# Kernel tuning notes

Hardware: AMD Instinct MI355X
Metric: run time of the kernel (lower is better)

## Reference

```python
import jax, jax.numpy as jnp
import numpy as np

N_QUBITS = 4
N_LAYERS = 3
N_FEATURES = 64
BATCH = 524288


def setup_inputs() -> dict:
    key = jax.random.key(0)
    k1, k2, k3, k4 = jax.random.split(key, 4)
    x = jax.random.normal(k1, (BATCH, N_FEATURES), jnp.float32)
    # nn.Linear(64, 4) params
    lim = 1.0 / np.sqrt(N_FEATURES)
    W_pre = jax.random.uniform(k2, (N_QUBITS, N_FEATURES), jnp.float32, -lim, lim)
    b_pre = jax.random.uniform(k3, (N_QUBITS,), jnp.float32, -lim, lim)
    # quantum circuit weights: randn * 0.1
    qweights = jax.random.normal(k4, (N_LAYERS, N_QUBITS, 2), jnp.float32) * 0.1
    return {"x": x, "W_pre": W_pre, "b_pre": b_pre, "qweights": qweights}


def _coef(theta, n):
    # reshape scalar or [B] angle to broadcast against [B, 2,..,2] (n-1 trailing dims after slicing)
    return jnp.reshape(theta, (-1,) + (1,) * (n - 1))


def _apply_ry(state, wire, theta):
    # RY(t) = [[cos t/2, -sin t/2], [sin t/2, cos t/2]] applied on `wire`
    n = state.ndim - 1
    s = jnp.moveaxis(state, 1 + wire, -1)
    a, b = s[..., 0], s[..., 1]
    c = _coef(jnp.cos(theta / 2), n)
    sn = _coef(jnp.sin(theta / 2), n)
    out = jnp.stack([c * a - sn * b, sn * a + c * b], axis=-1)
    return jnp.moveaxis(out, -1, 1 + wire)


def _apply_rz(state, wire, theta):
    # RZ(t) = diag(e^{-i t/2}, e^{+i t/2})
    n = state.ndim - 1
    s = jnp.moveaxis(state, 1 + wire, -1)
    half = _coef(theta / 2, n)
    out = jnp.stack([jnp.exp(-1j * half) * s[..., 0],
                     jnp.exp(1j * half) * s[..., 1]], axis=-1)
    return jnp.moveaxis(out, -1, 1 + wire)


def _apply_cnot(state, ctrl, tgt):
    s = jnp.moveaxis(state, (1 + ctrl, 1 + tgt), (-2, -1))
    s = jnp.concatenate([s[..., 0:1, :], s[..., 1:2, ::-1]], axis=-2)
    return jnp.moveaxis(s, (-2, -1), (1 + ctrl, 1 + tgt))


def _circuit(angles, qweights):
    # batched 4-qubit statevector simulation; state shape [B, 2,2,2,2] (wire 0 = MSB)
    B, n = angles.shape
    nl = qweights.shape[0]
    state = jnp.zeros((B,) + (2,) * n, jnp.complex64)
    state = state.at[(slice(None),) + (0,) * n].set(1.0)
    for w in range(n):
        state = _apply_ry(state, w, angles[:, w])
    for l in range(nl):
        for w in range(n):
            state = _apply_ry(state, w, qweights[l, w, 0])
            state = _apply_rz(state, w, qweights[l, w, 1])
        for w in range(n):
            state = _apply_cnot(state, w, (w + 1) % n)
    probs = state.real ** 2 + state.imag ** 2  # [B, 2,2,2,2] float32
    exps = []
    for w in range(n):
        marg = jnp.moveaxis(probs, 1 + w, 1).reshape(B, 2, -1).sum(-1)  # [B, 2]
        exps.append(marg[:, 0] - marg[:, 1])  # <Z_w>
    return jnp.stack(exps, axis=1)  # [B, n]


def reference(x, W_pre, b_pre, qweights):
    angles = jnp.tanh(x @ W_pre.T + b_pre)  # [B, n_qubits]
    return _circuit(angles, qweights).astype(jnp.float32)
```

## Files before the change

### kernel.cpp

```cpp
#include <hip/hip_runtime.h>
#include <cmath>


#define BAR() asm volatile("s_waitcnt lgkmcnt(0)\n\ts_barrier" ::: "memory")

#define LOADX(R0, R1, R2, R3, P, C)                       \
  R0 = xb[((P) * 256 + 0 * 64) * 16 + (C) * 4];           \
  R1 = xb[((P) * 256 + 1 * 64) * 16 + (C) * 4];           \
  R2 = xb[((P) * 256 + 2 * 64) * 16 + (C) * 4];           \
  R3 = xb[((P) * 256 + 3 * 64) * 16 + (C) * 4];

#define STAGE(R0, R1, R2, R3)                                            \
  *reinterpret_cast<float4*>(&lds[(0 * 64 + rrow) * XS + q4w]) = R0;     \
  *reinterpret_cast<float4*>(&lds[(1 * 64 + rrow) * XS + q4w]) = R1;     \
  *reinterpret_cast<float4*>(&lds[(2 * 64 + rrow) * XS + q4w]) = R2;     \
  *reinterpret_cast<float4*>(&lds[(3 * 64 + rrow) * XS + q4w]) = R3;

#define GEMV(A0, A1, A2, A3, C) {                                          \
  const float4 xv0 = *reinterpret_cast<const float4*>(&lds[tid * XS + 0]); \
  const float4 xv1 = *reinterpret_cast<const float4*>(&lds[tid * XS + 4]); \
  const float4 xv2 = *reinterpret_cast<const float4*>(&lds[tid * XS + 8]); \
  const float4 xv3 = *reinterpret_cast<const float4*>(&lds[tid * XS + 12]);\
  const float xr[16] = {xv0.x, xv0.y, xv0.z, xv0.w, xv1.x, xv1.y, xv1.z,   \
                        xv1.w, xv2.x, xv2.y, xv2.z, xv2.w, xv3.x, xv3.y,   \
                        xv3.z, xv3.w};                                     \
  _Pragma("unroll")                                                        \
  for (int f = 0; f < 16; ++f) {                                          \
    A0 = fmaf(xr[f], Wp[(C) * 16 + f], A0);                                \
    A1 = fmaf(xr[f], Wp[64 + (C) * 16 + f], A1);                           \
    A2 = fmaf(xr[f], Wp[128 + (C) * 16 + f], A2);                          \
    A3 = fmaf(xr[f], Wp[192 + (C) * 16 + f], A3);                          \
  } }

__global__ __launch_bounds__(256) void qprep_kernel(
    const float* __restrict__ qw,
    float* __restrict__ A_out)
{
  __shared__ float sre[16][17];
  __shared__ float sim[16][17];
  __shared__ float M[4][16][16];
  const int tid = threadIdx.x;
  const int col = tid >> 4;
  const int u   = tid & 15;

  sre[col][u] = (u == col) ? 1.0f : 0.0f;
  sim[col][u] = 0.0f;
  __syncthreads();

#pragma unroll
  for (int l = 0; l < 3; ++l) {
#pragma unroll
    for (int w = 0; w < 4; ++w) {
      const int mask = 8 >> w;
      float sh, ch, sh2, ch2;
      __sincosf(0.5f * qw[(l * 4 + w) * 2 + 0], &sh, &ch);
      __sincosf(0.5f * qw[(l * 4 + w) * 2 + 1], &sh2, &ch2);
      const int ua = u & ~mask, ub = u | mask;
      const float ar = sre[col][ua], ai = sim[col][ua];
      const float br = sre[col][ub], bi = sim[col][ub];
      __syncthreads();
      float nr, ni;
      if (u & mask) { nr = sh * ar + ch * br; ni = sh * ai + ch * bi; }
      else          { nr = ch * ar - sh * br; ni = ch * ai - sh * bi; }
      float rr, ri;
      if (u & mask) { rr = ch2 * nr - sh2 * ni; ri = ch2 * ni + sh2 * nr; }
      else          { rr = ch2 * nr + sh2 * ni; ri = ch2 * ni - sh2 * nr; }
      sre[col][u] = rr; sim[col][u] = ri;
      __syncthreads();
    }
    int src = u;
    if (src & 1) src ^= 8;
    if (src & 2) src ^= 1;
    if (src & 4) src ^= 2;
    if (src & 8) src ^= 4;
    const float pr = sre[col][src], pi = sim[col][src];
    __syncthreads();
    sre[col][u] = pr; sim[col][u] = pi;
    __syncthreads();
  }

  for (int idx = tid; idx < 1024; idx += 256) {
    const int w = idx >> 8, s = (idx >> 4) & 15, t = idx & 15;
    const int mask = 8 >> w;
    float acc = 0.0f;
#pragma unroll
    for (int uu = 0; uu < 16; ++uu) {
      const float z = (uu & mask) ? -1.0f : 1.0f;
      acc += z * (sre[s][uu] * sre[t][uu] + sim[s][uu] * sim[t][uu]);
    }
    M[w >> 0][s][t] = acc;
  }
  __syncthreads();

  for (int idx = tid; idx < 324; idx += 256) {
    const int w = idx & 3, pq = idx >> 2;
    const int p = pq / 9, q = pq % 9;
    const int i0 = p / 3, i1 = p % 3, i2 = q / 3, i3 = q % 3;
    float acc = 0.0f;
#pragma unroll
    for (int comb = 0; comb < 16; ++comb) {
      int s = 0, t = 0;
      float coef = 0.0625f;
      int j;
      j = (comb >> 3) & 1; s |= j << 3; t |= ((i0 == 2) ? (j ^ 1) : j) << 3; if (i0 == 1 && j) coef = -coef;
      j = (comb >> 2) & 1; s |= j << 2; t |= ((i1 == 2) ? (j ^ 1) : j) << 2; if (i1 == 1 && j) coef = -coef;
      j = (comb >> 1) & 1; s |= j << 1; t |= ((i2 == 2) ? (j ^ 1) : j) << 1; if (i2 == 1 && j) coef = -coef;
      j = comb & 1;        s |= j;      t |= ((i3 == 2) ? (j ^ 1) : j);      if (i3 == 1 && j) coef = -coef;
      acc = fmaf(coef, M[w][s][t], acc);
    }
    A_out[idx] = acc;
  }
}

__global__ __launch_bounds__(256)
__attribute__((amdgpu_waves_per_eu(4, 4)))
void qmain_kernel(
    const float* __restrict__ x,
    const float* __restrict__ Wp,
    const float* __restrict__ bp,
    const float4* __restrict__ Aws,
    float* __restrict__ out)
{
  constexpr int XS = 20;
  __shared__ alignas(16) float lds[256 * XS];

  const int tid = threadIdx.x;
  const size_t row0 = (size_t)blockIdx.x * 512;
  const int rrow = tid >> 2;
  const int q4w  = (tid & 3) << 2;
  const float4* xb = reinterpret_cast<const float4*>(x) +
                     (row0 + (size_t)rrow) * 16 + (tid & 3);

  float4 rbA0, rbA1, rbA2, rbA3, rbB0, rbB1, rbB2, rbB3;
  LOADX(rbA0, rbA1, rbA2, rbA3, 0, 0);
  LOADX(rbB0, rbB1, rbB2, rbB3, 0, 1);

  float aA0 = 0.f, aA1 = 0.f, aA2 = 0.f, aA3 = 0.f;
  float aB0 = 0.f, aB1 = 0.f, aB2 = 0.f, aB3 = 0.f;

  STAGE(rbA0, rbA1, rbA2, rbA3); LOADX(rbA0, rbA1, rbA2, rbA3, 0, 2); BAR();
  GEMV(aA0, aA1, aA2, aA3, 0);   BAR();
  STAGE(rbB0, rbB1, rbB2, rbB3); LOADX(rbB0, rbB1, rbB2, rbB3, 0, 3); BAR();
  GEMV(aA0, aA1, aA2, aA3, 1);   BAR();
  STAGE(rbA0, rbA1, rbA2, rbA3); LOADX(rbA0, rbA1, rbA2, rbA3, 1, 0); BAR();
  GEMV(aA0, aA1, aA2, aA3, 2);   BAR();
  STAGE(rbB0, rbB1, rbB2, rbB3); LOADX(rbB0, rbB1, rbB2, rbB3, 1, 1); BAR();
  GEMV(aA0, aA1, aA2, aA3, 3);   BAR();
  STAGE(rbA0, rbA1, rbA2, rbA3); LOADX(rbA0, rbA1, rbA2, rbA3, 1, 2); BAR();
  GEMV(aB0, aB1, aB2, aB3, 0);   BAR();
  STAGE(rbB0, rbB1, rbB2, rbB3); LOADX(rbB0, rbB1, rbB2, rbB3, 1, 3); BAR();
  GEMV(aB0, aB1, aB2, aB3, 1);   BAR();
  STAGE(rbA0, rbA1, rbA2, rbA3); BAR();
  GEMV(aB0, aB1, aB2, aB3, 2);   BAR();
  STAGE(rbB0, rbB1, rbB2, rbB3); BAR();
  GEMV(aB0, aB1, aB2, aB3, 3);

  float g0[9], h0[9], g1[9], h1[9];
  {
    const float t0 = 1.0f - 2.0f / (__expf(2.0f * (aA0 + bp[0])) + 1.0f);
    const float t1 = 1.0f - 2.0f / (__expf(2.0f * (aA1 + bp[1])) + 1.0f);
    const float t2 = 1.0f - 2.0f / (__expf(2.0f * (aA2 + bp[2])) + 1.0f);
    const float t3 = 1.0f - 2.0f / (__expf(2.0f * (aA3 + bp[3])) + 1.0f);
    float c0, s0, c1, s1, c2, s2, c3, s3;
    __sincosf(t0, &s0, &c0); __sincosf(t1, &s1, &c1);
    __sincosf(t2, &s2, &c2); __sincosf(t3, &s3, &c3);
    g0[0] = 1.f; g0[1] = c1; g0[2] = s1; g0[3] = c0; g0[4] = c0 * c1;
    g0[5] = c0 * s1; g0[6] = s0; g0[7] = s0 * c1; g0[8] = s0 * s1;
    h0[0] = 1.f; h0[1] = c3; h0[2] = s3; h0[3] = c2; h0[4] = c2 * c3;
    h0[5] = c2 * s3; h0[6] = s2; h0[7] = s2 * c3; h0[8] = s2 * s3;
  }
  {
    const float t0 = 1.0f - 2.0f / (__expf(2.0f * (aB0 + bp[0])) + 1.0f);
    const float t1 = 1.0f - 2.0f / (__expf(2.0f * (aB1 + bp[1])) + 1.0f);
    const float t2 = 1.0f - 2.0f / (__expf(2.0f * (aB2 + bp[2])) + 1.0f);
    const float t3 = 1.0f - 2.0f / (__expf(2.0f * (aB3 + bp[3])) + 1.0f);
    float c0, s0, c1, s1, c2, s2, c3, s3;
    __sincosf(t0, &s0, &c0); __sincosf(t1, &s1, &c1);
    __sincosf(t2, &s2, &c2); __sincosf(t3, &s3, &c3);
    g1[0] = 1.f; g1[1] = c1; g1[2] = s1; g1[3] = c0; g1[4] = c0 * c1;
    g1[5] = c0 * s1; g1[6] = s0; g1[7] = s0 * c1; g1[8] = s0 * s1;
    h1[0] = 1.f; h1[1] = c3; h1[2] = s3; h1[3] = c2; h1[4] = c2 * c3;
    h1[5] = c2 * s3; h1[6] = s2; h1[7] = s2 * c3; h1[8] = s2 * s3;
  }

  float e00 = 0.f, e01 = 0.f, e02 = 0.f, e03 = 0.f;
  float e10 = 0.f, e11 = 0.f, e12 = 0.f, e13 = 0.f;
#pragma unroll
  for (int p = 0; p < 9; ++p) {
#pragma unroll
    for (int q = 0; q < 9; ++q) {
      const float4 a4 = Aws[p * 9 + q];
      const float tA = g0[p] * h0[q];
      const float tB = g1[p] * h1[q];
      e00 = fmaf(a4.x, tA, e00); e01 = fmaf(a4.y, tA, e01);
      e02 = fmaf(a4.z, tA, e02); e03 = fmaf(a4.w, tA, e03);
      e10 = fmaf(a4.x, tB, e10); e11 = fmaf(a4.y, tB, e11);
      e12 = fmaf(a4.z, tB, e12); e13 = fmaf(a4.w, tB, e13);
    }
  }
  float4* out4 = reinterpret_cast<float4*>(out);
  out4[row0 + tid]       = make_float4(e00, e01, e02, e03);
  out4[row0 + 256 + tid] = make_float4(e10, e11, e12, e13);
}

extern "C" void kernel_launch(void* const* d_in, const int* in_sizes, int n_in,
                              void* d_out, int out_size, void* d_ws, size_t ws_size,
                              hipStream_t stream) {
  const float* x  = (const float*)d_in[0];
  const float* Wp = (const float*)d_in[1];
  const float* bp = (const float*)d_in[2];
  const float* qw = (const float*)d_in[3];
  float* out = (float*)d_out;
  float* A = (float*)d_ws;
  (void)n_in; (void)out_size; (void)ws_size;

  qprep_kernel<<<1, 256, 0, stream>>>(qw, A);

  const int B = in_sizes[0] / 64;
  qmain_kernel<<<B / 512, 256, 0, stream>>>(x, Wp, bp,
                                            (const float4*)A, out);
}
```

Baseline: 38.27 us.

## Fuse circuit-precompute into main kernel, recomputing per block in LDS

Removes the separate single-block prep kernel and has every block recompute the 16x16 unitary, the observable matrices and the 324-entry coefficient table in shared memory while its first x loads are in flight. The prefetch depth grows from two to three register buffers so that more global loads overlap the prep. This drops one kernel launch and the serial dependency between the two kernels. In exchange, every block does redundant prep work with about 14 barriers, and register pressure rises under the fixed waves-per-EU setting.

```diff
diff --git a/kernel.cpp b/kernel.cpp
--- a/kernel.cpp
+++ b/kernel.cpp
@@ -32,97 +32,21 @@
     A3 = fmaf(xr[f], Wp[192 + (C) * 16 + f], A3);                          \
   } }
 
-__global__ __launch_bounds__(256) void qprep_kernel(
-    const float* __restrict__ qw,
-    float* __restrict__ A_out)
-{
-  __shared__ float sre[16][17];
-  __shared__ float sim[16][17];
-  __shared__ float M[4][16][16];
-  const int tid = threadIdx.x;
-  const int col = tid >> 4;
-  const int u   = tid & 15;
-
-  sre[col][u] = (u == col) ? 1.0f : 0.0f;
-  sim[col][u] = 0.0f;
-  __syncthreads();
-
-#pragma unroll
-  for (int l = 0; l < 3; ++l) {
-#pragma unroll
-    for (int w = 0; w < 4; ++w) {
-      const int mask = 8 >> w;
-      float sh, ch, sh2, ch2;
-      __sincosf(0.5f * qw[(l * 4 + w) * 2 + 0], &sh, &ch);
-      __sincosf(0.5f * qw[(l * 4 + w) * 2 + 1], &sh2, &ch2);
-      const int ua = u & ~mask, ub = u | mask;
-      const float ar = sre[col][ua], ai = sim[col][ua];
-      const float br = sre[col][ub], bi = sim[col][ub];
-      __syncthreads();
-      float nr, ni;
-      if (u & mask) { nr = sh * ar + ch * br; ni = sh * ai + ch * bi; }
-      else          { nr = ch * ar - sh * br; ni = ch * ai - sh * bi; }
-      float rr, ri;
-      if (u & mask) { rr = ch2 * nr - sh2 * ni; ri = ch2 * ni + sh2 * nr; }
-      else          { rr = ch2 * nr + sh2 * ni; ri = ch2 * ni - sh2 * nr; }
-      sre[col][u] = rr; sim[col][u] = ri;
-      __syncthreads();
-    }
-    int src = u;
-    if (src & 1) src ^= 8;
-    if (src & 2) src ^= 1;
-    if (src & 4) src ^= 2;
-    if (src & 8) src ^= 4;
-    const float pr = sre[col][src], pi = sim[col][src];
-    __syncthreads();
-    sre[col][u] = pr; sim[col][u] = pi;
-    __syncthreads();
-  }
-
-  for (int idx = tid; idx < 1024; idx += 256) {
-    const int w = idx >> 8, s = (idx >> 4) & 15, t = idx & 15;
-    const int mask = 8 >> w;
-    float acc = 0.0f;
-#pragma unroll
-    for (int uu = 0; uu < 16; ++uu) {
-      const float z = (uu & mask) ? -1.0f : 1.0f;
-      acc += z * (sre[s][uu] * sre[t][uu] + sim[s][uu] * sim[t][uu]);
-    }
-    M[w >> 0][s][t] = acc;
-  }
-  __syncthreads();
-
-  for (int idx = tid; idx < 324; idx += 256) {
-    const int w = idx & 3, pq = idx >> 2;
-    const int p = pq / 9, q = pq % 9;
-    const int i0 = p / 3, i1 = p % 3, i2 = q / 3, i3 = q % 3;
-    float acc = 0.0f;
-#pragma unroll
-    for (int comb = 0; comb < 16; ++comb) {
-      int s = 0, t = 0;
-      float coef = 0.0625f;
-      int j;
-      j = (comb >> 3) & 1; s |= j << 3; t |= ((i0 == 2) ? (j ^ 1) : j) << 3; if (i0 == 1 && j) coef = -coef;
-      j = (comb >> 2) & 1; s |= j << 2; t |= ((i1 == 2) ? (j ^ 1) : j) << 2; if (i1 == 1 && j) coef = -coef;
-      j = (comb >> 1) & 1; s |= j << 1; t |= ((i2 == 2) ? (j ^ 1) : j) << 1; if (i2 == 1 && j) coef = -coef;
-      j = comb & 1;        s |= j;      t |= ((i3 == 2) ? (j ^ 1) : j);      if (i3 == 1 && j) coef = -coef;
-      acc = fmaf(coef, M[w][s][t], acc);
-    }
-    A_out[idx] = acc;
-  }
-}
-
 __global__ __launch_bounds__(256)
 __attribute__((amdgpu_waves_per_eu(4, 4)))
-void qmain_kernel(
+void qfused_kernel(
     const float* __restrict__ x,
     const float* __restrict__ Wp,
     const float* __restrict__ bp,
-    const float4* __restrict__ Aws,
+    const float* __restrict__ qw,
     float* __restrict__ out)
 {
-  constexpr int XS = 20;
-  __shared__ alignas(16) float lds[256 * XS];
+  constexpr int XS  = 20;
+  constexpr int AOF = 256 * XS;
+  __shared__ alignas(16) float lds[256 * XS + 324];
+  constexpr int SRE = 0;
+  constexpr int SIM = 272;
+  constexpr int MOF = 544;
 
   const int tid = threadIdx.x;
   const size_t row0 = (size_t)blockIdx.x * 512;
@@ -131,28 +55,105 @@
   const float4* xb = reinterpret_cast<const float4*>(x) +
                      (row0 + (size_t)rrow) * 16 + (tid & 3);
 
-  float4 rbA0, rbA1, rbA2, rbA3, rbB0, rbB1, rbB2, rbB3;
-  LOADX(rbA0, rbA1, rbA2, rbA3, 0, 0);
-  LOADX(rbB0, rbB1, rbB2, rbB3, 0, 1);
+  float4 rA0, rA1, rA2, rA3, rB0, rB1, rB2, rB3, rC0, rC1, rC2, rC3;
+  LOADX(rA0, rA1, rA2, rA3, 0, 0);
+  LOADX(rB0, rB1, rB2, rB3, 0, 1);
+  LOADX(rC0, rC1, rC2, rC3, 0, 2);
+
+  {
+    const int col = tid >> 4;
+    const int u   = tid & 15;
+    lds[SRE + col * 17 + u] = (u == col) ? 1.0f : 0.0f;
+    lds[SIM + col * 17 + u] = 0.0f;
+    BAR();
+
+#pragma unroll
+    for (int l = 0; l < 3; ++l) {
+#pragma unroll
+      for (int w = 0; w < 4; ++w) {
+        const int mask = 8 >> w;
+        float sh, ch, sh2, ch2;
+        __sincosf(0.5f * qw[(l * 4 + w) * 2 + 0], &sh, &ch);
+        __sincosf(0.5f * qw[(l * 4 + w) * 2 + 1], &sh2, &ch2);
+        const int ua = u & ~mask, ub = u | mask;
+        const float ar = lds[SRE + col * 17 + ua], ai = lds[SIM + col * 17 + ua];
+        const float br = lds[SRE + col * 17 + ub], bi = lds[SIM + col * 17 + ub];
+        BAR();
+        float nr, ni;
+        if (u & mask) { nr = sh * ar + ch * br; ni = sh * ai + ch * bi; }
+        else          { nr = ch * ar - sh * br; ni = ch * ai - sh * bi; }
+        float rr, ri;
+        if (u & mask) { rr = ch2 * nr - sh2 * ni; ri = ch2 * ni + sh2 * nr; }
+        else          { rr = ch2 * nr + sh2 * ni; ri = ch2 * ni - sh2 * nr; }
+        lds[SRE + col * 17 + u] = rr; lds[SIM + col * 17 + u] = ri;
+        BAR();
+      }
+      int src = u;
+      if (src & 1) src ^= 8;
+      if (src & 2) src ^= 1;
+      if (src & 4) src ^= 2;
+      if (src & 8) src ^= 4;
+      const float pr = lds[SRE + col * 17 + src], pi = lds[SIM + col * 17 + src];
+      BAR();
+      lds[SRE + col * 17 + u] = pr; lds[SIM + col * 17 + u] = pi;
+      BAR();
+    }
+
+#pragma unroll
+    for (int k = 0; k < 4; ++k) {
+      const int idx = tid + 256 * k;
+      const int w = idx >> 8, s = (idx >> 4) & 15, t = idx & 15;
+      const int mask = 8 >> w;
+      float acc = 0.0f;
+#pragma unroll
+      for (int uu = 0; uu < 16; ++uu) {
+        const float z = (uu & mask) ? -1.0f : 1.0f;
+        acc += z * (lds[SRE + s * 17 + uu] * lds[SRE + t * 17 + uu] +
+                    lds[SIM + s * 17 + uu] * lds[SIM + t * 17 + uu]);
+      }
+      lds[MOF + ((w * 16 + s) * 16 + t)] = acc;
+    }
+    BAR();
+
+    for (int idx = tid; idx < 324; idx += 256) {
+      const int w = idx & 3, pq = idx >> 2;
+      const int p = pq / 9, q = pq % 9;
+      const int i0 = p / 3, i1 = p % 3, i2 = q / 3, i3 = q % 3;
+      float acc = 0.0f;
+#pragma unroll
+      for (int comb = 0; comb < 16; ++comb) {
+        int s = 0, t = 0;
+        float coef = 0.0625f;
+        int j;
+        j = (comb >> 3) & 1; s |= j << 3; t |= ((i0 == 2) ? (j ^ 1) : j) << 3; if (i0 == 1 && j) coef = -coef;
+        j = (comb >> 2) & 1; s |= j << 2; t |= ((i1 == 2) ? (j ^ 1) : j) << 2; if (i1 == 1 && j) coef = -coef;
+        j = (comb >> 1) & 1; s |= j << 1; t |= ((i2 == 2) ? (j ^ 1) : j) << 1; if (i2 == 1 && j) coef = -coef;
+        j = comb & 1;        s |= j;      t |= ((i3 == 2) ? (j ^ 1) : j);      if (i3 == 1 && j) coef = -coef;
+        acc = fmaf(coef, lds[MOF + ((w * 16 + s) * 16 + t)], acc);
+      }
+      lds[AOF + idx] = acc;
+    }
+    BAR();
+  }
 
   float aA0 = 0.f, aA1 = 0.f, aA2 = 0.f, aA3 = 0.f;
   float aB0 = 0.f, aB1 = 0.f, aB2 = 0.f, aB3 = 0.f;
 
-  STAGE(rbA0, rbA1, rbA2, rbA3); LOADX(rbA0, rbA1, rbA2, rbA3, 0, 2); BAR();
-  GEMV(aA0, aA1, aA2, aA3, 0);   BAR();
-  STAGE(rbB0, rbB1, rbB2, rbB3); LOADX(rbB0, rbB1, rbB2, rbB3, 0, 3); BAR();
-  GEMV(aA0, aA1, aA2, aA3, 1);   BAR();
-  STAGE(rbA0, rbA1, rbA2, rbA3); LOADX(rbA0, rbA1, rbA2, rbA3, 1, 0); BAR();
-  GEMV(aA0, aA1, aA2, aA3, 2);   BAR();
-  STAGE(rbB0, rbB1, rbB2, rbB3); LOADX(rbB0, rbB1, rbB2, rbB3, 1, 1); BAR();
-  GEMV(aA0, aA1, aA2, aA3, 3);   BAR();
-  STAGE(rbA0, rbA1, rbA2, rbA3); LOADX(rbA0, rbA1, rbA2, rbA3, 1, 2); BAR();
-  GEMV(aB0, aB1, aB2, aB3, 0);   BAR();
-  STAGE(rbB0, rbB1, rbB2, rbB3); LOADX(rbB0, rbB1, rbB2, rbB3, 1, 3); BAR();
-  GEMV(aB0, aB1, aB2, aB3, 1);   BAR();
-  STAGE(rbA0, rbA1, rbA2, rbA3); BAR();
-  GEMV(aB0, aB1, aB2, aB3, 2);   BAR();
-  STAGE(rbB0, rbB1, rbB2, rbB3); BAR();
+  STAGE(rA0, rA1, rA2, rA3); LOADX(rA0, rA1, rA2, rA3, 0, 3); BAR();
+  GEMV(aA0, aA1, aA2, aA3, 0); BAR();
+  STAGE(rB0, rB1, rB2, rB3); LOADX(rB0, rB1, rB2, rB3, 1, 0); BAR();
+  GEMV(aA0, aA1, aA2, aA3, 1); BAR();
+  STAGE(rC0, rC1, rC2, rC3); LOADX(rC0, rC1, rC2, rC3, 1, 1); BAR();
+  GEMV(aA0, aA1, aA2, aA3, 2); BAR();
+  STAGE(rA0, rA1, rA2, rA3); LOADX(rA0, rA1, rA2, rA3, 1, 2); BAR();
+  GEMV(aA0, aA1, aA2, aA3, 3); BAR();
+  STAGE(rB0, rB1, rB2, rB3); LOADX(rB0, rB1, rB2, rB3, 1, 3); BAR();
+  GEMV(aB0, aB1, aB2, aB3, 0); BAR();
+  STAGE(rC0, rC1, rC2, rC3); BAR();
+  GEMV(aB0, aB1, aB2, aB3, 1); BAR();
+  STAGE(rA0, rA1, rA2, rA3); BAR();
+  GEMV(aB0, aB1, aB2, aB3, 2); BAR();
+  STAGE(rB0, rB1, rB2, rB3); BAR();
   GEMV(aB0, aB1, aB2, aB3, 3);
 
   float g0[9], h0[9], g1[9], h1[9];
@@ -189,7 +190,8 @@
   for (int p = 0; p < 9; ++p) {
 #pragma unroll
     for (int q = 0; q < 9; ++q) {
-      const float4 a4 = Aws[p * 9 + q];
+      const float4 a4 =
+          *reinterpret_cast<const float4*>(&lds[AOF + (p * 9 + q) * 4]);
       const float tA = g0[p] * h0[q];
       const float tB = g1[p] * h1[q];
       e00 = fmaf(a4.x, tA, e00); e01 = fmaf(a4.y, tA, e01);
@@ -211,12 +213,8 @@
   const float* bp = (const float*)d_in[2];
   const float* qw = (const float*)d_in[3];
   float* out = (float*)d_out;
-  float* A = (float*)d_ws;
-  (void)n_in; (void)out_size; (void)ws_size;
-
-  qprep_kernel<<<1, 256, 0, stream>>>(qw, A);
+  (void)d_ws; (void)ws_size; (void)n_in; (void)out_size;
 
   const int B = in_sizes[0] / 64;
-  qmain_kernel<<<B / 512, 256, 0, stream>>>(x, Wp, bp,
-                                            (const float4*)A, out);
+  qfused_kernel<<<B / 512, 256, 0, stream>>>(x, Wp, bp, qw, out);
 }
```

Result: no change. 38.07 us (-0.5%).
